# Optimization experiments

Hardware: AMD Instinct MI355X
Metric: run time of the kernel (lower is better)

The kernel has to match this reference:

```python
import jax, jax.numpy as jnp
import numpy as np

B, C, H, W = 8, 64, 256, 256
NUM_S = 256
S = 8 * NUM_S  # centers repeated for 8 neighbor offsets
TAU = 0.07
EPS = 1e-7


def _sample_ids():
    # Mirrors NeighborSample's index construction (randperm over interior pixels)
    rng = np.random.default_rng(0)
    s_ids = rng.permutation((H - 2) * (W - 2))[:NUM_S]
    ch = s_ids // (W - 2) + 1
    cw = s_ids % (W - 2) + 1
    c = ch * W + cw                      # center flat indices, [NUM_S]
    c_ids = np.tile(c, 8)                # [8*NUM_S]
    offsets = np.array([-(W + 1), -W, -(W - 1), -1, 1, W - 1, W, W + 1])
    delta = np.repeat(offsets, NUM_S)
    n_ids = c_ids + delta                # neighbor flat indices
    return c_ids.astype(np.int64), n_ids.astype(np.int64)


def setup_inputs() -> dict:
    key = jax.random.key(0)
    k1, k2, k3, k4 = jax.random.split(key, 4)
    c_ids, n_ids = _sample_ids()
    return {
        "f_q": jax.random.normal(k1, (B, C, H, W), dtype=jnp.float32),
        "f_k": jax.random.normal(k2, (B, C, H, W), dtype=jnp.float32),
        "W0": jax.random.normal(k3, (64, 64), dtype=jnp.float32) * 0.05,
        "b0": jnp.zeros((64,), dtype=jnp.float32),
        "W1": jax.random.normal(k4, (64, 16), dtype=jnp.float32) * 0.05,
        "b1": jnp.zeros((16,), dtype=jnp.float32),
        "c_ids": jnp.asarray(c_ids),
        "n_ids": jnp.asarray(n_ids),
    }


def _neighbor_sample(feat, c_ids, n_ids, W0, b0, W1, b1):
    b, c, h, w = feat.shape
    feat_r = feat.transpose(0, 2, 3, 1).reshape(b, h * w, c)  # [B, HW, C]
    feat_d = feat_r[:, c_ids, :] - feat_r[:, n_ids, :]        # gather diff, [B, S, C]
    feat_d = jax.nn.relu(feat_d @ W0 + b0) @ W1 + b1          # small MLP, [B, S, 16]
    feat_d = feat_d.transpose(0, 2, 1)                        # [B, 16, S]
    norm = jnp.sqrt(jnp.sum(feat_d * feat_d, axis=1, keepdims=True))
    return feat_d / (norm + EPS)                              # L2 normalize over channel dim


def reference(f_q, f_k, W0, b0, W1, b1, c_ids, n_ids):
    fq = _neighbor_sample(f_q, c_ids, n_ids, W0, b0, W1, b1)  # [B, 16, S]
    fk = jax.lax.stop_gradient(_neighbor_sample(f_k, c_ids, n_ids, W0, b0, W1, b1))
    # PatchNCE loss
    l_pos = jnp.sum(fk * fq, axis=1)[:, :, None]              # [B, S, 1]
    l_neg = jnp.einsum('bcs,bct->bst', fq, fk)                # [B, S, S]
    eye = jnp.eye(S, dtype=bool)[None, :, :]
    l_neg = jnp.where(eye, -jnp.inf, l_neg)
    logits = jnp.concatenate([l_pos, l_neg], axis=2) / TAU    # [B, S, S+1]
    logits = logits.reshape(-1, S + 1)
    # cross entropy with target class 0 for every row
    loss = jnp.mean(jax.nn.logsumexp(logits, axis=-1) - logits[:, 0])
    return loss
```

## Files before the change

### kernel.cpp

```cpp
#include <hip/hip_runtime.h>
#include <math.h>

#define HWSZ 65536
#define SDIM 2048
#define NCHUNK 8
#define CHUNKSZ 256
#define INV_TAU 14.285714285714286f
#define EPSN 1e-7f

__global__ __launch_bounds__(256) void feat_kernel(
    const float* __restrict__ f_q, const float* __restrict__ f_k,
    const float* __restrict__ W0, const float* __restrict__ b0,
    const float* __restrict__ W1, const float* __restrict__ b1,
    const int* __restrict__ c_ids, const int* __restrict__ n_ids,
    float* __restrict__ Fq, float* __restrict__ Fk)
{
    __shared__ float sd[4][64];
    __shared__ float sh[4][64];
    const int w    = threadIdx.x >> 6;
    const int lane = threadIdx.x & 63;
    const int row  = blockIdx.x * 4 + w;
    const int which = row >> 14;
    const int r = row & 16383;
    const int b = r >> 11;
    const int s = r & 2047;

    const float* feat = which ? f_k : f_q;
    const int cid = c_ids[s];
    const int nid = n_ids[s];
    const float* base = feat + ((size_t)(b * 64 + lane)) * HWSZ;
    float d = base[cid] - base[nid];
    sd[w][lane] = d;
    __syncthreads();

    float acc = b0[lane];
    #pragma unroll 16
    for (int c = 0; c < 64; ++c)
        acc = fmaf(sd[w][c], W0[c * 64 + lane], acc);
    sh[w][lane] = fmaxf(acc, 0.0f);
    __syncthreads();

    if (lane < 16) {
        float o = b1[lane];
        #pragma unroll 16
        for (int j = 0; j < 64; ++j)
            o = fmaf(sh[w][j], W1[j * 16 + lane], o);
        float s2 = o * o;
        s2 += __shfl_xor(s2, 1, 16);
        s2 += __shfl_xor(s2, 2, 16);
        s2 += __shfl_xor(s2, 4, 16);
        s2 += __shfl_xor(s2, 8, 16);
        float val = o / (sqrtf(s2) + EPSN);
        float* F = which ? Fk : Fq;
        F[((size_t)(b * SDIM + s)) * 16 + lane] = val;
    }
}

__global__ __launch_bounds__(256) void gram_kernel(
    const float* __restrict__ Fq, const float* __restrict__ Fk,
    float* __restrict__ partial, float* __restrict__ diag)
{
    const int s     = blockIdx.x * 256 + threadIdx.x;
    const int chunk = blockIdx.y;
    const int b     = blockIdx.z;

    const float4* q4 = (const float4*)(Fq + ((size_t)(b * SDIM + s)) * 16);
    const float4 qa = q4[0], qb = q4[1], qc = q4[2], qd = q4[3];
    const float* fk = Fk + (size_t)b * SDIM * 16;

    float sum_e = 0.0f;
    float dsave = 0.0f;
    const int t0 = chunk * CHUNKSZ;
    for (int t = t0; t < t0 + CHUNKSZ; ++t) {
        const float4* k4 = (const float4*)(fk + (size_t)t * 16);
        const float4 ka = k4[0], kb = k4[1], kc = k4[2], kd = k4[3];
        float dot = qa.x * ka.x;
        dot = fmaf(qa.y, ka.y, dot); dot = fmaf(qa.z, ka.z, dot); dot = fmaf(qa.w, ka.w, dot);
        dot = fmaf(qb.x, kb.x, dot); dot = fmaf(qb.y, kb.y, dot); dot = fmaf(qb.z, kb.z, dot); dot = fmaf(qb.w, kb.w, dot);
        dot = fmaf(qc.x, kc.x, dot); dot = fmaf(qc.y, kc.y, dot); dot = fmaf(qc.z, kc.z, dot); dot = fmaf(qc.w, kc.w, dot);
        dot = fmaf(qd.x, kd.x, dot); dot = fmaf(qd.y, kd.y, dot); dot = fmaf(qd.z, kd.z, dot); dot = fmaf(qd.w, kd.w, dot);
        sum_e += __expf(fmaf(dot, INV_TAU, -INV_TAU));
        if (t == s) dsave = dot;
    }
    partial[((size_t)(b * SDIM + s)) * NCHUNK + chunk] = sum_e;
    if (chunk == (s >> 8)) diag[b * SDIM + s] = dsave;
}

__global__ __launch_bounds__(256) void loss_kernel(
    const float* __restrict__ partial, const float* __restrict__ diag,
    float* __restrict__ out)
{
    const int idx = blockIdx.x * 256 + threadIdx.x;
    float tot = 0.0f;
    #pragma unroll
    for (int c = 0; c < NCHUNK; ++c) tot += partial[(size_t)idx * NCHUNK + c];
    float loss = INV_TAU + logf(tot) - diag[idx] * INV_TAU;

    loss += __shfl_xor(loss, 32, 64);
    loss += __shfl_xor(loss, 16, 64);
    loss += __shfl_xor(loss, 8, 64);
    loss += __shfl_xor(loss, 4, 64);
    loss += __shfl_xor(loss, 2, 64);
    loss += __shfl_xor(loss, 1, 64);

    __shared__ float wsum[4];
    const int lane = threadIdx.x & 63, w = threadIdx.x >> 6;
    if (lane == 0) wsum[w] = loss;
    __syncthreads();
    if (threadIdx.x == 0) {
        float blk = wsum[0] + wsum[1] + wsum[2] + wsum[3];
        atomicAdd(out, blk * (1.0f / 16384.0f));
    }
}

extern "C" void kernel_launch(void* const* d_in, const int* in_sizes, int n_in,
                              void* d_out, int out_size, void* d_ws, size_t ws_size,
                              hipStream_t stream) {
    const float* f_q   = (const float*)d_in[0];
    const float* f_k   = (const float*)d_in[1];
    const float* W0    = (const float*)d_in[2];
    const float* b0    = (const float*)d_in[3];
    const float* W1    = (const float*)d_in[4];
    const float* b1    = (const float*)d_in[5];
    const int*   c_ids = (const int*)d_in[6];
    const int*   n_ids = (const int*)d_in[7];

    float* ws      = (float*)d_ws;
    float* Fq      = ws;
    float* Fk      = Fq + 262144;
    float* partial = Fk + 262144;
    float* diag    = partial + 131072;
    float* out     = (float*)d_out;

    hipMemsetAsync(d_out, 0, sizeof(float), stream);
    feat_kernel<<<8192, 256, 0, stream>>>(f_q, f_k, W0, b0, W1, b1, c_ids, n_ids, Fq, Fk);
    gram_kernel<<<dim3(SDIM / 256, NCHUNK, 8), 256, 0, stream>>>(Fq, Fk, partial, diag);
    loss_kernel<<<64, 256, 0, stream>>>(partial, diag, out);
}
```

Baseline: 325.7 us.

## Process all eight neighbors per center in one wave and split gram into more chunks

The feature kernel now has each wave handle one center and all 8 of its neighbor offsets. The center value is loaded once and W0 is reused across 8 rows in registers, so the grid shrinks from 8192 to 1024 blocks. The gram kernel splits the key dimension into 32 chunks of 64 instead of 8 chunks of 256, giving more blocks and parallelism, and partial sums are stored chunk-major so the loss kernel reads them coalesced. The costs are more partial sums to write and reduce, and higher register use in the feature kernel.

```diff
diff --git a/kernel.cpp b/kernel.cpp
--- a/kernel.cpp
+++ b/kernel.cpp
@@ -3,8 +3,9 @@
 
 #define HWSZ 65536
 #define SDIM 2048
-#define NCHUNK 8
-#define CHUNKSZ 256
+#define NCENT 256
+#define NCHUNK 32
+#define CHUNKSZ 64
 #define INV_TAU 14.285714285714286f
 #define EPSN 1e-7f
 
@@ -15,44 +16,58 @@
     const int* __restrict__ c_ids, const int* __restrict__ n_ids,
     float* __restrict__ Fq, float* __restrict__ Fk)
 {
-    __shared__ float sd[4][64];
-    __shared__ float sh[4][64];
+    __shared__ float sd[4][8][65];
+    __shared__ float sh[4][8][65];
     const int w    = threadIdx.x >> 6;
     const int lane = threadIdx.x & 63;
     const int row  = blockIdx.x * 4 + w;
-    const int which = row >> 14;
-    const int r = row & 16383;
-    const int b = r >> 11;
-    const int s = r & 2047;
+    const int which = row >> 11;
+    const int r = row & 2047;
+    const int b = r >> 8;
+    const int cidx = r & 255;
 
     const float* feat = which ? f_k : f_q;
-    const int cid = c_ids[s];
-    const int nid = n_ids[s];
+    const int cid = c_ids[cidx];
     const float* base = feat + ((size_t)(b * 64 + lane)) * HWSZ;
-    float d = base[cid] - base[nid];
-    sd[w][lane] = d;
+    const float cval = base[cid];
+    #pragma unroll
+    for (int k = 0; k < 8; ++k) {
+        const int nid = n_ids[cidx + 256 * k];
+        sd[w][k][lane] = cval - base[nid];
+    }
     __syncthreads();
 
-    float acc = b0[lane];
-    #pragma unroll 16
-    for (int c = 0; c < 64; ++c)
-        acc = fmaf(sd[w][c], W0[c * 64 + lane], acc);
-    sh[w][lane] = fmaxf(acc, 0.0f);
+    float acc[8];
+    #pragma unroll
+    for (int k = 0; k < 8; ++k) acc[k] = b0[lane];
+    for (int c = 0; c < 64; ++c) {
+        const float w0 = W0[c * 64 + lane];
+        #pragma unroll
+        for (int k = 0; k < 8; ++k)
+            acc[k] = fmaf(sd[w][k][c], w0, acc[k]);
+    }
+    #pragma unroll
+    for (int k = 0; k < 8; ++k) sh[w][k][lane] = fmaxf(acc[k], 0.0f);
     __syncthreads();
 
-    if (lane < 16) {
-        float o = b1[lane];
+    const int i  = lane & 15;
+    const int k0 = lane >> 4;
+    float* F = which ? Fk : Fq;
+    #pragma unroll
+    for (int p = 0; p < 2; ++p) {
+        const int k = p * 4 + k0;
+        float o = b1[i];
         #pragma unroll 16
         for (int j = 0; j < 64; ++j)
-            o = fmaf(sh[w][j], W1[j * 16 + lane], o);
+            o = fmaf(sh[w][k][j], W1[j * 16 + i], o);
         float s2 = o * o;
         s2 += __shfl_xor(s2, 1, 16);
         s2 += __shfl_xor(s2, 2, 16);
         s2 += __shfl_xor(s2, 4, 16);
         s2 += __shfl_xor(s2, 8, 16);
-        float val = o / (sqrtf(s2) + EPSN);
-        float* F = which ? Fk : Fq;
-        F[((size_t)(b * SDIM + s)) * 16 + lane] = val;
+        const float val = o / (sqrtf(s2) + EPSN);
+        const int s = cidx + 256 * k;
+        F[((size_t)(b * SDIM + s)) * 16 + i] = val;
     }
 }
 
@@ -71,6 +86,7 @@
     float sum_e = 0.0f;
     float dsave = 0.0f;
     const int t0 = chunk * CHUNKSZ;
+    #pragma unroll 2
     for (int t = t0; t < t0 + CHUNKSZ; ++t) {
         const float4* k4 = (const float4*)(fk + (size_t)t * 16);
         const float4 ka = k4[0], kb = k4[1], kc = k4[2], kd = k4[3];
@@ -82,8 +98,8 @@
         sum_e += __expf(fmaf(dot, INV_TAU, -INV_TAU));
         if (t == s) dsave = dot;
     }
-    partial[((size_t)(b * SDIM + s)) * NCHUNK + chunk] = sum_e;
-    if (chunk == (s >> 8)) diag[b * SDIM + s] = dsave;
+    partial[(size_t)chunk * 16384 + b * SDIM + s] = sum_e;
+    if (chunk == (s >> 6)) diag[b * SDIM + s] = dsave;
 }
 
 __global__ __launch_bounds__(256) void loss_kernel(
@@ -93,7 +109,7 @@
     const int idx = blockIdx.x * 256 + threadIdx.x;
     float tot = 0.0f;
     #pragma unroll
-    for (int c = 0; c < NCHUNK; ++c) tot += partial[(size_t)idx * NCHUNK + c];
+    for (int c = 0; c < NCHUNK; ++c) tot += partial[(size_t)c * 16384 + idx];
     float loss = INV_TAU + logf(tot) - diag[idx] * INV_TAU;
 
     loss += __shfl_xor(loss, 32, 64);
@@ -129,11 +145,11 @@
     float* Fq      = ws;
     float* Fk      = Fq + 262144;
     float* partial = Fk + 262144;
-    float* diag    = partial + 131072;
+    float* diag    = partial + 524288;
     float* out     = (float*)d_out;
 
     hipMemsetAsync(d_out, 0, sizeof(float), stream);
-    feat_kernel<<<8192, 256, 0, stream>>>(f_q, f_k, W0, b0, W1, b1, c_ids, n_ids, Fq, Fk);
+    feat_kernel<<<1024, 256, 0, stream>>>(f_q, f_k, W0, b0, W1, b1, c_ids, n_ids, Fq, Fk);
     gram_kernel<<<dim3(SDIM / 256, NCHUNK, 8), 256, 0, stream>>>(Fq, Fk, partial, diag);
     loss_kernel<<<64, 256, 0, stream>>>(partial, diag, out);
 }
```

Result: faster. 292.7 us (-10.1%).
